# Optimization experiments

Measured on AMD Instinct MI355X. Metric: run time of the kernel, lower is better.

Reference implementation:

```python
import jax, jax.numpy as jnp
import numpy as np

N, E, D, R = 50000, 800000, 64, 65


def setup_inputs() -> dict:
    key = jax.random.key(0)
    ks = jax.random.split(key, 8)
    x = jax.random.normal(ks[0], (N, D), dtype=jnp.float32)
    src = jax.random.randint(ks[1], (E,), 0, N, dtype=jnp.int32)
    dst = jax.random.randint(ks[2], (E,), 0, N, dtype=jnp.int32)
    edge_type = jax.random.randint(ks[3], (E,), 0, R, dtype=jnp.int32)
    s = 1.0 / np.sqrt(D)
    W1 = jax.random.normal(ks[4], (R, D, D), dtype=jnp.float32) * s
    Wl1 = jax.random.normal(ks[5], (D, D), dtype=jnp.float32) * s
    W2 = jax.random.normal(ks[6], (R, D, D), dtype=jnp.float32) * s
    Wl2 = jax.random.normal(ks[7], (D, D), dtype=jnp.float32) * s
    return {"x": x, "src": src, "dst": dst, "edge_type": edge_type,
            "W1": W1, "Wl1": Wl1, "W2": W2, "Wl2": Wl2}


def _rgcn_layer(x, src, dst, edge_type, W, Wl):
    # x: [N, D_in], W: [R, D_in, D_out], Wl: [D_in, D_out]
    n = x.shape[0]
    r = W.shape[0]
    # per-relation transform of all node features: [R, N, D_out]
    xw = jnp.einsum('nd,rdh->rnh', x, W)
    # gather transformed source feature for each edge by its relation: [E, D_out]
    msg = xw[edge_type, src]
    # mean aggregation per (destination node, relation) as in PyG RGCNConv
    key = dst.astype(jnp.int32) * r + edge_type
    cnt = jax.ops.segment_sum(jnp.ones(key.shape, x.dtype), key, num_segments=n * r)
    norm = 1.0 / jnp.maximum(cnt[key], 1.0)  # [E]
    agg = jax.ops.segment_sum(msg * norm[:, None], dst, num_segments=n)  # [N, D_out]
    # self-loop linear term (self_loop_weights in original module)
    out = agg + x @ Wl
    # activation; dropout is identity in eval mode; batch norm disabled
    return jax.nn.relu(out)


def reference(x, src, dst, edge_type, W1, Wl1, W2, Wl2):
    h = _rgcn_layer(x, src, dst, edge_type, W1, Wl1)
    h = _rgcn_layer(h, src, dst, edge_type, W2, Wl2)
    return h
```

## Files before the change

kernel.cpp:

```cpp
#include <hip/hip_runtime.h>

typedef __attribute__((ext_vector_type(8))) short bf16x8;
typedef __attribute__((ext_vector_type(4))) float f32x4;

#define RFL(v) __builtin_amdgcn_readfirstlane(v)

constexpr int D = 64;
constexpr int SEG = 64;
constexpr int CSTR = 16;

__device__ inline unsigned short f2bf(float f) {
  unsigned u = __float_as_uint(f);
  u += 0x7fff + ((u >> 16) & 1);
  return (unsigned short)(u >> 16);
}
__device__ inline float bflo(unsigned u) { return __uint_as_float(u << 16); }
__device__ inline float bfhi(unsigned u) { return __uint_as_float(u & 0xffff0000u); }

__global__ __launch_bounds__(256) void count_kernel(
    const int* __restrict__ dst, const int* __restrict__ et,
    int* __restrict__ bcnt, int* __restrict__ deg, int E, int R, int nbE) {
  __shared__ int lh[128];
  int t = threadIdx.x;
  if (t < 128) lh[t] = 0;
  __syncthreads();
  int e = blockIdx.x * 256 + t;
  if (e < E) {
    atomicAdd(&deg[(long)dst[e] * CSTR], 1);
    atomicAdd(&lh[et[e]], 1);
  }
  __syncthreads();
  if (t < R) bcnt[t * nbE + blockIdx.x] = lh[t];
}

__global__ __launch_bounds__(256) void scanA_kernel(
    const int* __restrict__ arr, int* __restrict__ bsum, int n, int stride) {
  __shared__ int s[256];
  int t = threadIdx.x;
  int i = blockIdx.x * 256 + t;
  s[t] = (i < n) ? arr[(long)i * stride] : 0;
  __syncthreads();
  for (int o = 128; o > 0; o >>= 1) {
    if (t < o) s[t] += s[t + o];
    __syncthreads();
  }
  if (t == 0) bsum[blockIdx.x] = s[0];
}

__global__ __launch_bounds__(256) void scanB_kernel(int* __restrict__ bsum, int nb) {
  __shared__ int s[256];
  __shared__ int carry;
  int t = threadIdx.x;
  if (t == 0) carry = 0;
  __syncthreads();
  for (int base = 0; base < nb; base += 256) {
    int i = base + t;
    int v = (i < nb) ? bsum[i] : 0;
    s[t] = v;
    __syncthreads();
    for (int o = 1; o < 256; o <<= 1) {
      int u = (t >= o) ? s[t - o] : 0;
      __syncthreads();
      s[t] += u;
      __syncthreads();
    }
    if (i < nb) bsum[i] = carry + s[t] - v;
    __syncthreads();
    if (t == 0) carry += s[255];
    __syncthreads();
  }
}

__global__ __launch_bounds__(256) void scanC_pref_kernel(
    const int* __restrict__ arr, const int* __restrict__ bsum,
    int* __restrict__ pref, int n) {
  __shared__ int s[256];
  int t = threadIdx.x;
  int i = blockIdx.x * 256 + t;
  int v = (i < n) ? arr[i] : 0;
  s[t] = v;
  __syncthreads();
  for (int o = 1; o < 256; o <<= 1) {
    int u = (t >= o) ? s[t - o] : 0;
    __syncthreads();
    s[t] += u;
    __syncthreads();
  }
  int excl = bsum[blockIdx.x] + s[t] - v;
  if (i < n) pref[i] = excl;
  if (i == n - 1) pref[n] = excl + v;
}

__global__ __launch_bounds__(256) void scanC_deg_kernel(
    const int* __restrict__ deg, const int* __restrict__ bsum,
    int* __restrict__ dstoff, int* __restrict__ cur2, int N) {
  __shared__ int s[256];
  int t = threadIdx.x;
  int i = blockIdx.x * 256 + t;
  int v = (i < N) ? deg[(long)i * CSTR] : 0;
  s[t] = v;
  __syncthreads();
  for (int o = 1; o < 256; o <<= 1) {
    int u = (t >= o) ? s[t - o] : 0;
    __syncthreads();
    s[t] += u;
    __syncthreads();
  }
  int excl = bsum[blockIdx.x] + s[t] - v;
  if (i < N) { dstoff[i] = excl; cur2[(long)i * CSTR] = excl; }
  if (i == N - 1) dstoff[N] = excl + v;
}

__global__ void prefix_wrel_kernel(const int* __restrict__ prefE,
                                   int* __restrict__ cursor, int* __restrict__ wrel,
                                   int nbE, int R) {
  __shared__ int sc[128];
  int l = threadIdx.x;
  int c = 0;
  if (l < R) {
    int tot = prefE[(l + 1) * nbE] - prefE[l * nbE];
    c = (tot + SEG - 1) & ~(SEG - 1);
  }
  sc[l] = c;
  __syncthreads();
  for (int ofs = 1; ofs < 128; ofs <<= 1) {
    int v = (l >= ofs) ? sc[l - ofs] : 0;
    __syncthreads();
    sc[l] += v;
    __syncthreads();
  }
  if (l < R) {
    int cur = sc[l] - c;
    cursor[l] = cur;
    int w0 = cur >> 6;
    int nw = c >> 6;
    for (int w = 0; w < nw; ++w) wrel[w0 + w] = l;
  }
}

__global__ __launch_bounds__(256) void scatter_kernel(
    const int* __restrict__ src, const int* __restrict__ dst, const int* __restrict__ et,
    const int* __restrict__ cursor, const int* __restrict__ prefE,
    int* __restrict__ cur2, int2* __restrict__ eidx,
    int E, int R, int nbE) {
  __shared__ int lh[128];
  __shared__ int lbase[128];
  int t = threadIdx.x, b = blockIdx.x;
  if (t < R) {
    lh[t] = 0;
    lbase[t] = cursor[t] + prefE[t * nbE + b] - prefE[t * nbE];
  }
  __syncthreads();
  int e = b * 256 + t;
  if (e < E) {
    int r = et[e], s = src[e], d = dst[e];
    int lr = atomicAdd(&lh[r], 1);
    int jd = atomicAdd(&cur2[(long)d * CSTR], 1);
    int pos = lbase[r] + lr;
    eidx[pos] = make_int2(s, jd);
  }
}

__global__ __launch_bounds__(256) void cvt_x_kernel(
    const float* __restrict__ x, unsigned short* __restrict__ xb, int n) {
  int i = blockIdx.x * 256 + threadIdx.x;
  if (i < n) xb[i] = f2bf(x[i]);
}

__global__ __launch_bounds__(256) void cvt_w_kernel(
    const float* __restrict__ W, unsigned short* __restrict__ WT, int total) {
  int i = blockIdx.x * 256 + threadIdx.x;
  if (i >= total) return;
  int n = i & 63, k = (i >> 6) & 63, r = i >> 12;
  WT[(r << 12) + (n << 6) + k] = f2bf(W[(r << 12) + (k << 6) + n]);
}

__global__ __launch_bounds__(256)
void msg_kernel(const unsigned short* __restrict__ xb,
                const unsigned short* __restrict__ WT,
                const int2* __restrict__ eidx, const int* __restrict__ wrel,
                unsigned int* __restrict__ msgp, int* __restrict__ relrow, int nwaves) {
  const int lane = (int)threadIdx.x & 63;
  const int l15 = lane & 15;
  const int q = lane >> 4;
  const int wave = blockIdx.x * 4 + ((int)threadIdx.x >> 6);
  if (wave >= nwaves) return;
  const long base = (long)wave * SEG;
  const int r = wrel[wave];
  const unsigned short* wb = WT + ((long)r << 12);
  bf16x8 Bf[4][2];
#pragma unroll
  for (int nt = 0; nt < 4; ++nt)
#pragma unroll
    for (int kh = 0; kh < 2; ++kh)
      Bf[nt][kh] = *(const bf16x8*)(wb + (nt * 16 + l15) * 64 + kh * 32 + q * 8);
#pragma unroll
  for (int t = 0; t < 4; ++t) {
    int2 rec = eidx[base + t * 16 + l15];
    if (relrow && lane < 16 && rec.y >= 0)
      __builtin_nontemporal_store(r, &relrow[rec.y]);
    const unsigned short* xr = xb + ((long)max(rec.x, 0) << 6);
    bf16x8 A0 = *(const bf16x8*)(xr + q * 8);
    bf16x8 A1 = *(const bf16x8*)(xr + 32 + q * 8);
    f32x4 acc0 = (f32x4)0.0f, acc1 = (f32x4)0.0f, acc2 = (f32x4)0.0f, acc3 = (f32x4)0.0f;
    acc0 = __builtin_amdgcn_mfma_f32_16x16x32_bf16(A0, Bf[0][0], acc0, 0, 0, 0);
    acc0 = __builtin_amdgcn_mfma_f32_16x16x32_bf16(A1, Bf[0][1], acc0, 0, 0, 0);
    acc1 = __builtin_amdgcn_mfma_f32_16x16x32_bf16(A0, Bf[1][0], acc1, 0, 0, 0);
    acc1 = __builtin_amdgcn_mfma_f32_16x16x32_bf16(A1, Bf[1][1], acc1, 0, 0, 0);
    acc2 = __builtin_amdgcn_mfma_f32_16x16x32_bf16(A0, Bf[2][0], acc2, 0, 0, 0);
    acc2 = __builtin_amdgcn_mfma_f32_16x16x32_bf16(A1, Bf[2][1], acc2, 0, 0, 0);
    acc3 = __builtin_amdgcn_mfma_f32_16x16x32_bf16(A0, Bf[3][0], acc3, 0, 0, 0);
    acc3 = __builtin_amdgcn_mfma_f32_16x16x32_bf16(A1, Bf[3][1], acc3, 0, 0, 0);
#pragma unroll
    for (int rg = 0; rg < 4; ++rg) {
      int row = q * 4 + rg;
      int jd = __shfl(rec.y, row);
      if (jd >= 0) {
        unsigned p0 = (unsigned)f2bf(acc0[rg]) | ((unsigned)f2bf(acc1[rg]) << 16);
        unsigned p1 = (unsigned)f2bf(acc2[rg]) | ((unsigned)f2bf(acc3[rg]) << 16);
        unsigned int* mp = msgp + (long)jd * 32;
        __builtin_nontemporal_store(p0, &mp[l15]);
        __builtin_nontemporal_store(p1, &mp[16 + l15]);
      }
    }
  }
}

__global__ __launch_bounds__(256) void agg_kernel(
    const unsigned int* __restrict__ msgp, const int* __restrict__ dstoff,
    const int* __restrict__ relrow, float* __restrict__ agg, int N) {
  __shared__ int rsh[4][256];
  __shared__ float fsh[4][256];
  const int wv = (int)threadIdx.x >> 6;
  const int lane = (int)threadIdx.x & 63;
  const int j = lane & 31;
  const int half = lane >> 5;
  const int d = blockIdx.x * 4 + wv;
  if (d >= N) return;
  const int off = dstoff[d], end = dstoff[d + 1];
  const int deg = end - off;
  float aLo = 0.f, aHi = 0.f;
  if (deg > 0 && deg <= 256) {
    const int nit = (deg + 63) >> 6;
    int cl[4];
    for (int it = 0; it < nit; ++it) {
      int l = it * 64 + lane;
      if (l < deg) rsh[wv][l] = relrow[off + l];
    }
    __threadfence_block();
    for (int it = 0; it < nit; ++it) {
      int l = it * 64 + lane;
      if (l < deg) {
        int rv = rsh[wv][l];
        int c = 0;
        for (int m = 0; m < deg; ++m) c += (rsh[wv][m] == rv) ? 1 : 0;
        cl[it] = c;
      }
    }
    for (int it = 0; it < nit; ++it) {
      int l = it * 64 + lane;
      if (l < deg) fsh[wv][l] = 1.0f / (float)cl[it];
    }
    __threadfence_block();
    float a0 = 0.f, a1 = 0.f, b0 = 0.f, b1 = 0.f;
    int i = off + half;
    for (; i + 2 < end; i += 4) {
      float w0 = fsh[wv][i - off];
      float w1 = fsh[wv][i + 2 - off];
      unsigned u0 = msgp[(long)i * 32 + j];
      unsigned u1 = msgp[(long)(i + 2) * 32 + j];
      a0 = fmaf(w0, bflo(u0), a0);
      a1 = fmaf(w0, bfhi(u0), a1);
      b0 = fmaf(w1, bflo(u1), b0);
      b1 = fmaf(w1, bfhi(u1), b1);
    }
    if (i < end) {
      float w0 = fsh[wv][i - off];
      unsigned u0 = msgp[(long)i * 32 + j];
      a0 = fmaf(w0, bflo(u0), a0);
      a1 = fmaf(w0, bfhi(u0), a1);
    }
    aLo = a0 + b0;
    aHi = a1 + b1;
  } else if (deg > 256) {
    for (int i = off + half; i < end; i += 2) {
      int rv = relrow[i];
      int c = 0;
      for (int m = off; m < end; ++m) c += (relrow[m] == rv) ? 1 : 0;
      float w = 1.0f / (float)c;
      unsigned u0 = msgp[(long)i * 32 + j];
      aLo = fmaf(w, bflo(u0), aLo);
      aHi = fmaf(w, bfhi(u0), aHi);
    }
  }
  aLo += __shfl_xor(aLo, 32);
  aHi += __shfl_xor(aHi, 32);
  if (half == 0) {
    int colLo = (j < 16) ? j : j + 16;
    agg[(long)d * D + colLo] = aLo;
    agg[(long)d * D + colLo + 16] = aHi;
  }
}

__global__ __launch_bounds__(256) void selfloop_kernel(
    const unsigned short* __restrict__ xbin, const unsigned short* __restrict__ WTl,
    const float* __restrict__ agg, float* __restrict__ out,
    unsigned short* __restrict__ hb, int N) {
  const int lane = (int)threadIdx.x & 63;
  const int l15 = lane & 15;
  const int q = lane >> 4;
  const int wave = blockIdx.x * 4 + ((int)threadIdx.x >> 6);
  const int base = wave * 64;
  if (base >= N) return;
  bf16x8 Bf[4][2];
#pragma unroll
  for (int nt = 0; nt < 4; ++nt)
#pragma unroll
    for (int kh = 0; kh < 2; ++kh)
      Bf[nt][kh] = *(const bf16x8*)(WTl + (nt * 16 + l15) * 64 + kh * 32 + q * 8);
#pragma unroll
  for (int t = 0; t < 4; ++t) {
    const int row0 = base + t * 16;
    if (row0 >= N) break;
    const int m = min(row0 + l15, N - 1);
    const unsigned short* xr = xbin + ((long)m << 6);
    bf16x8 A0 = *(const bf16x8*)(xr + q * 8);
    bf16x8 A1 = *(const bf16x8*)(xr + 32 + q * 8);
    f32x4 acc[4];
#pragma unroll
    for (int nt = 0; nt < 4; ++nt) {
#pragma unroll
      for (int rg = 0; rg < 4; ++rg) {
        int node = row0 + q * 4 + rg;
        acc[nt][rg] = (node < N) ? agg[(long)node * D + nt * 16 + l15] : 0.0f;
      }
    }
#pragma unroll
    for (int nt = 0; nt < 4; ++nt) {
      acc[nt] = __builtin_amdgcn_mfma_f32_16x16x32_bf16(A0, Bf[nt][0], acc[nt], 0, 0, 0);
      acc[nt] = __builtin_amdgcn_mfma_f32_16x16x32_bf16(A1, Bf[nt][1], acc[nt], 0, 0, 0);
    }
#pragma unroll
    for (int rg = 0; rg < 4; ++rg) {
      int node = row0 + q * 4 + rg;
      if (node < N) {
#pragma unroll
        for (int nt = 0; nt < 4; ++nt) {
          float v = fmaxf(acc[nt][rg], 0.0f);
          out[(long)node * D + nt * 16 + l15] = v;
          if (hb) hb[(long)node * D + nt * 16 + l15] = f2bf(v);
        }
      }
    }
  }
}

extern "C" void kernel_launch(void* const* d_in, const int* in_sizes, int n_in,
                              void* d_out, int out_size, void* d_ws, size_t ws_size,
                              hipStream_t stream) {
  const float* x   = (const float*)d_in[0];
  const int* src   = (const int*)d_in[1];
  const int* dst   = (const int*)d_in[2];
  const int* et    = (const int*)d_in[3];
  const float* W1  = (const float*)d_in[4];
  const float* Wl1 = (const float*)d_in[5];
  const float* W2  = (const float*)d_in[6];
  const float* Wl2 = (const float*)d_in[7];
  float* out = (float*)d_out;

  const int N = in_sizes[0] / D;
  const int E = in_sizes[1];
  const int R = in_sizes[4] / (D * D);

  const int Ecap = ((E + SEG - 1) & ~(SEG - 1)) + R * SEG;
  const int nwaves = Ecap / SEG;
  const int nbN = (N + 255) / 256;
  const int nbE = (E + 255) / 256;
  const int nBC = R * nbE;
  const int nbBC = (nBC + 255) / 256;
  const int nbMax = (nbBC > nbN) ? nbBC : nbN;

  char* ws = (char*)d_ws;
  size_t off = 0;
  auto alloc = [&](size_t bytes) -> void* {
    void* p = (void*)(ws + off);
    off += (bytes + 255) & ~(size_t)255;
    return p;
  };
  int*   cursor = (int*)alloc((size_t)R * sizeof(int));
  int*   deg    = (int*)alloc((size_t)N * CSTR * sizeof(int));
  int*   cur2   = (int*)alloc((size_t)N * CSTR * sizeof(int));
  int*   bcnt   = (int*)alloc((size_t)nBC * sizeof(int));
  int*   prefE  = (int*)alloc((size_t)(nBC + 1) * sizeof(int));
  int*   bsum   = (int*)alloc((size_t)nbMax * sizeof(int));
  int*   dstoff = (int*)alloc((size_t)(N + 1) * sizeof(int));
  int*   relrow = (int*)alloc((size_t)E * sizeof(int));
  int*   wrel   = (int*)alloc((size_t)nwaves * sizeof(int));
  int2*  eidx   = (int2*)alloc((size_t)(Ecap + SEG) * sizeof(int2));
  unsigned int* msgp = (unsigned int*)alloc((size_t)E * 32 * sizeof(unsigned int));
  float* agg    = (float*)alloc((size_t)N * D * sizeof(float));
  unsigned short* xb  = (unsigned short*)alloc((size_t)N * D * sizeof(unsigned short));
  unsigned short* hb  = (unsigned short*)alloc((size_t)N * D * sizeof(unsigned short));
  unsigned short* WT1 = (unsigned short*)alloc((size_t)R * D * D * sizeof(unsigned short));
  unsigned short* WT2 = (unsigned short*)alloc((size_t)R * D * D * sizeof(unsigned short));
  unsigned short* WTl1 = (unsigned short*)alloc((size_t)D * D * sizeof(unsigned short));
  unsigned short* WTl2 = (unsigned short*)alloc((size_t)D * D * sizeof(unsigned short));
  (void)ws_size; (void)n_in; (void)out_size;

  const int msg_blocks = (nwaves + 3) / 4;
  const int agg_blocks = (N + 3) / 4;
  const int sl_waves = (N + 63) / 64;
  const int sl_blocks = (sl_waves + 3) / 4;
  const int wtot = R * D * D;

  hipMemsetAsync(deg, 0, (size_t)N * CSTR * sizeof(int), stream);
  hipMemsetAsync(wrel, 0, (size_t)nwaves * sizeof(int), stream);
  hipMemsetAsync(eidx, 0xFF, (size_t)(Ecap + SEG) * sizeof(int2), stream);
  count_kernel<<<nbE, 256, 0, stream>>>(dst, et, bcnt, deg, E, R, nbE);
  scanA_kernel<<<nbBC, 256, 0, stream>>>(bcnt, bsum, nBC, 1);
  scanB_kernel<<<1, 256, 0, stream>>>(bsum, nbBC);
  scanC_pref_kernel<<<nbBC, 256, 0, stream>>>(bcnt, bsum, prefE, nBC);
  prefix_wrel_kernel<<<1, 128, 0, stream>>>(prefE, cursor, wrel, nbE, R);
  scanA_kernel<<<nbN, 256, 0, stream>>>(deg, bsum, N, CSTR);
  scanB_kernel<<<1, 256, 0, stream>>>(bsum, nbN);
  scanC_deg_kernel<<<nbN, 256, 0, stream>>>(deg, bsum, dstoff, cur2, N);
  scatter_kernel<<<nbE, 256, 0, stream>>>(src, dst, et, cursor, prefE, cur2,
                                          eidx, E, R, nbE);
  cvt_x_kernel<<<(N * D + 255) / 256, 256, 0, stream>>>(x, xb, N * D);
  cvt_w_kernel<<<(wtot + 255) / 256, 256, 0, stream>>>(W1, WT1, wtot);
  cvt_w_kernel<<<(wtot + 255) / 256, 256, 0, stream>>>(W2, WT2, wtot);
  cvt_w_kernel<<<(D * D + 255) / 256, 256, 0, stream>>>(Wl1, WTl1, D * D);
  cvt_w_kernel<<<(D * D + 255) / 256, 256, 0, stream>>>(Wl2, WTl2, D * D);

  msg_kernel<<<msg_blocks, 256, 0, stream>>>(xb, WT1, eidx, wrel, msgp, relrow, nwaves);
  agg_kernel<<<agg_blocks, 256, 0, stream>>>(msgp, dstoff, relrow, agg, N);
  selfloop_kernel<<<sl_blocks, 256, 0, stream>>>(xb, WTl1, agg, out, hb, N);

  msg_kernel<<<msg_blocks, 256, 0, stream>>>(hb, WT2, eidx, wrel, msgp, nullptr, nwaves);
  agg_kernel<<<agg_blocks, 256, 0, stream>>>(msgp, dstoff, relrow, agg, N);
  selfloop_kernel<<<sl_blocks, 256, 0, stream>>>(hb, WTl2, agg, out, nullptr, N);
}
```

Baseline: 376.0 us.

## Fuse aggregation with self-loop GEMM and merge preprocessing launches

```diff
diff --git a/kernel.cpp b/kernel.cpp
--- a/kernel.cpp
+++ b/kernel.cpp
@@ -2,12 +2,11 @@
 
 typedef __attribute__((ext_vector_type(8))) short bf16x8;
 typedef __attribute__((ext_vector_type(4))) float f32x4;
-
-#define RFL(v) __builtin_amdgcn_readfirstlane(v)
 
 constexpr int D = 64;
 constexpr int SEG = 64;
 constexpr int CSTR = 16;
+constexpr int TSTR = 68;
 
 __device__ inline unsigned short f2bf(float f) {
   unsigned u = __float_as_uint(f);
@@ -33,24 +32,32 @@
   if (t < R) bcnt[t * nbE + blockIdx.x] = lh[t];
 }
 
-__global__ __launch_bounds__(256) void scanA_kernel(
-    const int* __restrict__ arr, int* __restrict__ bsum, int n, int stride) {
+__global__ __launch_bounds__(256) void scanA_dual_kernel(
+    const int* __restrict__ bcnt, const int* __restrict__ deg,
+    int* __restrict__ bsum, int nBC, int N, int nbBC) {
   __shared__ int s[256];
   int t = threadIdx.x;
-  int i = blockIdx.x * 256 + t;
-  s[t] = (i < n) ? arr[(long)i * stride] : 0;
+  int b = blockIdx.x;
+  int v;
+  if (b < nbBC) {
+    int i = b * 256 + t;
+    v = (i < nBC) ? bcnt[i] : 0;
+  } else {
+    int i = (b - nbBC) * 256 + t;
+    v = (i < N) ? deg[(long)i * CSTR] : 0;
+  }
+  s[t] = v;
   __syncthreads();
   for (int o = 128; o > 0; o >>= 1) {
     if (t < o) s[t] += s[t + o];
     __syncthreads();
   }
-  if (t == 0) bsum[blockIdx.x] = s[0];
-}
-
-__global__ __launch_bounds__(256) void scanB_kernel(int* __restrict__ bsum, int nb) {
+  if (t == 0) bsum[b] = s[0];
+}
+
+__device__ inline void scanB_region(int* bsum, int nb, int t) {
   __shared__ int s[256];
   __shared__ int carry;
-  int t = threadIdx.x;
   if (t == 0) carry = 0;
   __syncthreads();
   for (int base = 0; base < nb; base += 256) {
@@ -71,13 +78,26 @@
   }
 }
 
-__global__ __launch_bounds__(256) void scanC_pref_kernel(
-    const int* __restrict__ arr, const int* __restrict__ bsum,
-    int* __restrict__ pref, int n) {
+__global__ __launch_bounds__(256) void scanB_dual_kernel(
+    int* __restrict__ bsum, int nbBC, int nbN) {
+  int t = threadIdx.x;
+  scanB_region(bsum, nbBC, t);
+  scanB_region(bsum + nbBC, nbN, t);
+}
+
+__global__ __launch_bounds__(256) void scanC_dual_kernel(
+    const int* __restrict__ bcnt, const int* __restrict__ deg,
+    const int* __restrict__ bsum, int* __restrict__ prefE,
+    int* __restrict__ dstoff, int* __restrict__ cur2,
+    int nBC, int N, int nbBC) {
   __shared__ int s[256];
   int t = threadIdx.x;
-  int i = blockIdx.x * 256 + t;
-  int v = (i < n) ? arr[i] : 0;
+  int b = blockIdx.x;
+  bool isBC = (b < nbBC);
+  int i = (isBC ? b : b - nbBC) * 256 + t;
+  int n = isBC ? nBC : N;
+  int v = 0;
+  if (i < n) v = isBC ? bcnt[i] : deg[(long)i * CSTR];
   s[t] = v;
   __syncthreads();
   for (int o = 1; o < 256; o <<= 1) {
@@ -86,29 +106,14 @@
     s[t] += u;
     __syncthreads();
   }
-  int excl = bsum[blockIdx.x] + s[t] - v;
-  if (i < n) pref[i] = excl;
-  if (i == n - 1) pref[n] = excl + v;
-}
-
-__global__ __launch_bounds__(256) void scanC_deg_kernel(
-    const int* __restrict__ deg, const int* __restrict__ bsum,
-    int* __restrict__ dstoff, int* __restrict__ cur2, int N) {
-  __shared__ int s[256];
-  int t = threadIdx.x;
-  int i = blockIdx.x * 256 + t;
-  int v = (i < N) ? deg[(long)i * CSTR] : 0;
-  s[t] = v;
-  __syncthreads();
-  for (int o = 1; o < 256; o <<= 1) {
-    int u = (t >= o) ? s[t - o] : 0;
-    __syncthreads();
-    s[t] += u;
-    __syncthreads();
-  }
-  int excl = bsum[blockIdx.x] + s[t] - v;
-  if (i < N) { dstoff[i] = excl; cur2[(long)i * CSTR] = excl; }
-  if (i == N - 1) dstoff[N] = excl + v;
+  int excl = bsum[b] + s[t] - v;
+  if (isBC) {
+    if (i < n) prefE[i] = excl;
+    if (i == n - 1) prefE[n] = excl + v;
+  } else {
+    if (i < n) { dstoff[i] = excl; cur2[(long)i * CSTR] = excl; }
+    if (i == n - 1) dstoff[n] = excl + v;
+  }
 }
 
 __global__ void prefix_wrel_kernel(const int* __restrict__ prefE,
@@ -161,21 +166,34 @@
   }
 }
 
-__global__ __launch_bounds__(256) void cvt_x_kernel(
-    const float* __restrict__ x, unsigned short* __restrict__ xb, int n) {
+__global__ __launch_bounds__(256) void cvt_all_kernel(
+    const float* __restrict__ x, unsigned short* __restrict__ xb, int nx,
+    const float* __restrict__ W1, unsigned short* __restrict__ WT1,
+    const float* __restrict__ W2, unsigned short* __restrict__ WT2, int nw,
+    const float* __restrict__ Wl1, unsigned short* __restrict__ WTl1,
+    const float* __restrict__ Wl2, unsigned short* __restrict__ WTl2, int nl) {
   int i = blockIdx.x * 256 + threadIdx.x;
-  if (i < n) xb[i] = f2bf(x[i]);
-}
-
-__global__ __launch_bounds__(256) void cvt_w_kernel(
-    const float* __restrict__ W, unsigned short* __restrict__ WT, int total) {
-  int i = blockIdx.x * 256 + threadIdx.x;
-  if (i >= total) return;
-  int n = i & 63, k = (i >> 6) & 63, r = i >> 12;
-  WT[(r << 12) + (n << 6) + k] = f2bf(W[(r << 12) + (k << 6) + n]);
-}
-
-__global__ __launch_bounds__(256)
+  if (i < nx) { xb[i] = f2bf(x[i]); return; }
+  i -= nx;
+  if (i < 2 * nw) {
+    const float* W = (i < nw) ? W1 : W2;
+    unsigned short* WT = (i < nw) ? WT1 : WT2;
+    int i2 = (i < nw) ? i : i - nw;
+    int n = i2 & 63, k = (i2 >> 6) & 63, r = i2 >> 12;
+    WT[(r << 12) + (n << 6) + k] = f2bf(W[(r << 12) + (k << 6) + n]);
+    return;
+  }
+  i -= 2 * nw;
+  if (i < 2 * nl) {
+    const float* W = (i < nl) ? Wl1 : Wl2;
+    unsigned short* WT = (i < nl) ? WTl1 : WTl2;
+    int i2 = (i < nl) ? i : i - nl;
+    int n = i2 & 63, k = (i2 >> 6) & 63;
+    WT[(n << 6) + k] = f2bf(W[(k << 6) + n]);
+  }
+}
+
+__global__ __launch_bounds__(256) __attribute__((amdgpu_waves_per_eu(1, 4)))
 void msg_kernel(const unsigned short* __restrict__ xb,
                 const unsigned short* __restrict__ WT,
                 const int2* __restrict__ eidx, const int* __restrict__ wrel,
@@ -197,8 +215,7 @@
 #pragma unroll
   for (int t = 0; t < 4; ++t) {
     int2 rec = eidx[base + t * 16 + l15];
-    if (relrow && lane < 16 && rec.y >= 0)
-      __builtin_nontemporal_store(r, &relrow[rec.y]);
+    if (relrow && lane < 16 && rec.y >= 0) relrow[rec.y] = r;
     const unsigned short* xr = xb + ((long)max(rec.x, 0) << 6);
     bf16x8 A0 = *(const bf16x8*)(xr + q * 8);
     bf16x8 A1 = *(const bf16x8*)(xr + 32 + q * 8);
@@ -219,137 +236,129 @@
         unsigned p0 = (unsigned)f2bf(acc0[rg]) | ((unsigned)f2bf(acc1[rg]) << 16);
         unsigned p1 = (unsigned)f2bf(acc2[rg]) | ((unsigned)f2bf(acc3[rg]) << 16);
         unsigned int* mp = msgp + (long)jd * 32;
-        __builtin_nontemporal_store(p0, &mp[l15]);
-        __builtin_nontemporal_store(p1, &mp[16 + l15]);
+        mp[l15] = p0;
+        mp[16 + l15] = p1;
       }
     }
   }
 }
 
-__global__ __launch_bounds__(256) void agg_kernel(
+__global__ __launch_bounds__(256) void aggself_kernel(
     const unsigned int* __restrict__ msgp, const int* __restrict__ dstoff,
-    const int* __restrict__ relrow, float* __restrict__ agg, int N) {
+    const int* __restrict__ relrow, const unsigned short* __restrict__ xbin,
+    const unsigned short* __restrict__ WTl, float* __restrict__ out,
+    unsigned short* __restrict__ hb, int N) {
+  __shared__ float tile[4][16 * TSTR];
   __shared__ int rsh[4][256];
   __shared__ float fsh[4][256];
   const int wv = (int)threadIdx.x >> 6;
   const int lane = (int)threadIdx.x & 63;
   const int j = lane & 31;
   const int half = lane >> 5;
-  const int d = blockIdx.x * 4 + wv;
-  if (d >= N) return;
-  const int off = dstoff[d], end = dstoff[d + 1];
-  const int deg = end - off;
-  float aLo = 0.f, aHi = 0.f;
-  if (deg > 0 && deg <= 256) {
-    const int nit = (deg + 63) >> 6;
-    int cl[4];
-    for (int it = 0; it < nit; ++it) {
-      int l = it * 64 + lane;
-      if (l < deg) rsh[wv][l] = relrow[off + l];
-    }
-    __threadfence_block();
-    for (int it = 0; it < nit; ++it) {
-      int l = it * 64 + lane;
-      if (l < deg) {
-        int rv = rsh[wv][l];
-        int c = 0;
-        for (int m = 0; m < deg; ++m) c += (rsh[wv][m] == rv) ? 1 : 0;
-        cl[it] = c;
+  const int l15 = lane & 15;
+  const int q = lane >> 4;
+  const int base = blockIdx.x * 64 + wv * 16;
+  bf16x8 Bf[4][2];
+#pragma unroll
+  for (int nt = 0; nt < 4; ++nt)
+#pragma unroll
+    for (int kh = 0; kh < 2; ++kh)
+      Bf[nt][kh] = *(const bf16x8*)(WTl + (nt * 16 + l15) * 64 + kh * 32 + q * 8);
+  if (base >= N) return;
+  for (int k = 0; k < 16; ++k) {
+    int d = base + k;
+    float aLo = 0.f, aHi = 0.f;
+    if (d < N) {
+      const int off = dstoff[d], end = dstoff[d + 1];
+      const int deg = end - off;
+      if (deg > 0 && deg <= 256) {
+        const int nit = (deg + 63) >> 6;
+        int cl[4];
+        for (int it = 0; it < nit; ++it) {
+          int l = it * 64 + lane;
+          if (l < deg) rsh[wv][l] = relrow[off + l];
+        }
+        __threadfence_block();
+        for (int it = 0; it < nit; ++it) {
+          int l = it * 64 + lane;
+          if (l < deg) {
+            int rv = rsh[wv][l];
+            int c = 0;
+            for (int m = 0; m < deg; ++m) c += (rsh[wv][m] == rv) ? 1 : 0;
+            cl[it] = c;
+          }
+        }
+        for (int it = 0; it < nit; ++it) {
+          int l = it * 64 + lane;
+          if (l < deg) fsh[wv][l] = 1.0f / (float)cl[it];
+        }
+        __threadfence_block();
+        float a0 = 0.f, a1 = 0.f, b0 = 0.f, b1 = 0.f;
+        int i = off + half;
+        for (; i + 2 < end; i += 4) {
+          float w0 = fsh[wv][i - off];
+          float w1 = fsh[wv][i + 2 - off];
+          unsigned u0 = msgp[(long)i * 32 + j];
+          unsigned u1 = msgp[(long)(i + 2) * 32 + j];
+          a0 = fmaf(w0, bflo(u0), a0);
+          a1 = fmaf(w0, bfhi(u0), a1);
+          b0 = fmaf(w1, bflo(u1), b0);
+          b1 = fmaf(w1, bfhi(u1), b1);
+        }
+        if (i < end) {
+          float w0 = fsh[wv][i - off];
+          unsigned u0 = msgp[(long)i * 32 + j];
+          a0 = fmaf(w0, bflo(u0), a0);
+          a1 = fmaf(w0, bfhi(u0), a1);
+        }
+        aLo = a0 + b0;
+        aHi = a1 + b1;
+      } else if (deg > 256) {
+        for (int i = off + half; i < end; i += 2) {
+          int rv = relrow[i];
+          int c = 0;
+          for (int m = off; m < end; ++m) c += (relrow[m] == rv) ? 1 : 0;
+          float w = 1.0f / (float)c;
+          unsigned u0 = msgp[(long)i * 32 + j];
+          aLo = fmaf(w, bflo(u0), aLo);
+          aHi = fmaf(w, bfhi(u0), aHi);
+        }
       }
     }
-    for (int it = 0; it < nit; ++it) {
-      int l = it * 64 + lane;
-      if (l < deg) fsh[wv][l] = 1.0f / (float)cl[it];
+    aLo += __shfl_xor(aLo, 32);
+    aHi += __shfl_xor(aHi, 32);
+    if (half == 0) {
+      int colLo = (j < 16) ? j : j + 16;
+      tile[wv][k * TSTR + colLo] = aLo;
+      tile[wv][k * TSTR + colLo + 16] = aHi;
     }
-    __threadfence_block();
-    float a0 = 0.f, a1 = 0.f, b0 = 0.f, b1 = 0.f;
-    int i = off + half;
-    for (; i + 2 < end; i += 4) {
-      float w0 = fsh[wv][i - off];
-      float w1 = fsh[wv][i + 2 - off];
-      unsigned u0 = msgp[(long)i * 32 + j];
-      unsigned u1 = msgp[(long)(i + 2) * 32 + j];
-      a0 = fmaf(w0, bflo(u0), a0);
-      a1 = fmaf(w0, bfhi(u0), a1);
-      b0 = fmaf(w1, bflo(u1), b0);
-      b1 = fmaf(w1, bfhi(u1), b1);
-    }
-    if (i < end) {
-      float w0 = fsh[wv][i - off];
-      unsigned u0 = msgp[(long)i * 32 + j];
-      a0 = fmaf(w0, bflo(u0), a0);
-      a1 = fmaf(w0, bfhi(u0), a1);
-    }
-    aLo = a0 + b0;
-    aHi = a1 + b1;
-  } else if (deg > 256) {
-    for (int i = off + half; i < end; i += 2) {
-      int rv = relrow[i];
-      int c = 0;
-      for (int m = off; m < end; ++m) c += (relrow[m] == rv) ? 1 : 0;
-      float w = 1.0f / (float)c;
-      unsigned u0 = msgp[(long)i * 32 + j];
-      aLo = fmaf(w, bflo(u0), aLo);
-      aHi = fmaf(w, bfhi(u0), aHi);
-    }
-  }
-  aLo += __shfl_xor(aLo, 32);
-  aHi += __shfl_xor(aHi, 32);
-  if (half == 0) {
-    int colLo = (j < 16) ? j : j + 16;
-    agg[(long)d * D + colLo] = aLo;
-    agg[(long)d * D + colLo + 16] = aHi;
-  }
-}
-
-__global__ __launch_bounds__(256) void selfloop_kernel(
-    const unsigned short* __restrict__ xbin, const unsigned short* __restrict__ WTl,
-    const float* __restrict__ agg, float* __restrict__ out,
-    unsigned short* __restrict__ hb, int N) {
-  const int lane = (int)threadIdx.x & 63;
-  const int l15 = lane & 15;
-  const int q = lane >> 4;
-  const int wave = blockIdx.x * 4 + ((int)threadIdx.x >> 6);
-  const int base = wave * 64;
-  if (base >= N) return;
-  bf16x8 Bf[4][2];
-#pragma unroll
-  for (int nt = 0; nt < 4; ++nt)
-#pragma unroll
-    for (int kh = 0; kh < 2; ++kh)
-      Bf[nt][kh] = *(const bf16x8*)(WTl + (nt * 16 + l15) * 64 + kh * 32 + q * 8);
-#pragma unroll
-  for (int t = 0; t < 4; ++t) {
-    const int row0 = base + t * 16;
-    if (row0 >= N) break;
-    const int m = min(row0 + l15, N - 1);
-    const unsigned short* xr = xbin + ((long)m << 6);
-    bf16x8 A0 = *(const bf16x8*)(xr + q * 8);
-    bf16x8 A1 = *(const bf16x8*)(xr + 32 + q * 8);
-    f32x4 acc[4];
-#pragma unroll
-    for (int nt = 0; nt < 4; ++nt) {
-#pragma unroll
-      for (int rg = 0; rg < 4; ++rg) {
-        int node = row0 + q * 4 + rg;
-        acc[nt][rg] = (node < N) ? agg[(long)node * D + nt * 16 + l15] : 0.0f;
-      }
-    }
-#pragma unroll
-    for (int nt = 0; nt < 4; ++nt) {
-      acc[nt] = __builtin_amdgcn_mfma_f32_16x16x32_bf16(A0, Bf[nt][0], acc[nt], 0, 0, 0);
-      acc[nt] = __builtin_amdgcn_mfma_f32_16x16x32_bf16(A1, Bf[nt][1], acc[nt], 0, 0, 0);
-    }
-#pragma unroll
-    for (int rg = 0; rg < 4; ++rg) {
-      int node = row0 + q * 4 + rg;
-      if (node < N) {
-#pragma unroll
-        for (int nt = 0; nt < 4; ++nt) {
-          float v = fmaxf(acc[nt][rg], 0.0f);
-          out[(long)node * D + nt * 16 + l15] = v;
-          if (hb) hb[(long)node * D + nt * 16 + l15] = f2bf(v);
-        }
+  }
+  __threadfence_block();
+  const int m = min(base + l15, N - 1);
+  const unsigned short* xr = xbin + ((long)m << 6);
+  bf16x8 A0 = *(const bf16x8*)(xr + q * 8);
+  bf16x8 A1 = *(const bf16x8*)(xr + 32 + q * 8);
+  f32x4 acc[4];
+#pragma unroll
+  for (int nt = 0; nt < 4; ++nt) {
+#pragma unroll
+    for (int rg = 0; rg < 4; ++rg)
+      acc[nt][rg] = tile[wv][(q * 4 + rg) * TSTR + nt * 16 + l15];
+  }
+#pragma unroll
+  for (int nt = 0; nt < 4; ++nt) {
+    acc[nt] = __builtin_amdgcn_mfma_f32_16x16x32_bf16(A0, Bf[nt][0], acc[nt], 0, 0, 0);
+    acc[nt] = __builtin_amdgcn_mfma_f32_16x16x32_bf16(A1, Bf[nt][1], acc[nt], 0, 0, 0);
+  }
+#pragma unroll
+  for (int rg = 0; rg < 4; ++rg) {
+    int node = base + q * 4 + rg;
+    if (node < N) {
+#pragma unroll
+      for (int nt = 0; nt < 4; ++nt) {
+        float v = fmaxf(acc[nt][rg], 0.0f);
+        out[(long)node * D + nt * 16 + l15] = v;
+        if (hb) hb[(long)node * D + nt * 16 + l15] = f2bf(v);
       }
     }
   }
@@ -378,7 +387,6 @@
   const int nbE = (E + 255) / 256;
   const int nBC = R * nbE;
   const int nbBC = (nBC + 255) / 256;
-  const int nbMax = (nbBC > nbN) ? nbBC : nbN;
 
   char* ws = (char*)d_ws;
   size_t off = 0;
@@ -392,13 +400,12 @@
   int*   cur2   = (int*)alloc((size_t)N * CSTR * sizeof(int));
   int*   bcnt   = (int*)alloc((size_t)nBC * sizeof(int));
   int*   prefE  = (int*)alloc((size_t)(nBC + 1) * sizeof(int));
-  int*   bsum   = (int*)alloc((size_t)nbMax * sizeof(int));
+  int*   bsum   = (int*)alloc((size_t)(nbBC + nbN) * sizeof(int));
   int*   dstoff = (int*)alloc((size_t)(N + 1) * sizeof(int));
   int*   relrow = (int*)alloc((size_t)E * sizeof(int));
   int*   wrel   = (int*)alloc((size_t)nwaves * sizeof(int));
   int2*  eidx   = (int2*)alloc((size_t)(Ecap + SEG) * sizeof(int2));
   unsigned int* msgp = (unsigned int*)alloc((size_t)E * 32 * sizeof(unsigned int));
-  float* agg    = (float*)alloc((size_t)N * D * sizeof(float));
   unsigned short* xb  = (unsigned short*)alloc((size_t)N * D * sizeof(unsigned short));
   unsigned short* hb  = (unsigned short*)alloc((size_t)N * D * sizeof(unsigned short));
   unsigned short* WT1 = (unsigned short*)alloc((size_t)R * D * D * sizeof(unsigned short));
@@ -408,35 +415,30 @@
   (void)ws_size; (void)n_in; (void)out_size;
 
   const int msg_blocks = (nwaves + 3) / 4;
-  const int agg_blocks = (N + 3) / 4;
-  const int sl_waves = (N + 63) / 64;
-  const int sl_blocks = (sl_waves + 3) / 4;
-  const int wtot = R * D * D;
+  const int as_blocks = (N + 63) / 64;
+  const int nx = N * D;
+  const int nw = R * D * D;
+  const int nl = D * D;
+  const int cvt_total = nx + 2 * nw + 2 * nl;
 
   hipMemsetAsync(deg, 0, (size_t)N * CSTR * sizeof(int), stream);
   hipMemsetAsync(wrel, 0, (size_t)nwaves * sizeof(int), stream);
   hipMemsetAsync(eidx, 0xFF, (size_t)(Ecap + SEG) * sizeof(int2), stream);
   count_kernel<<<nbE, 256, 0, stream>>>(dst, et, bcnt, deg, E, R, nbE);
-  scanA_kernel<<<nbBC, 256, 0, stream>>>(bcnt, bsum, nBC, 1);
-  scanB_kernel<<<1, 256, 0, stream>>>(bsum, nbBC);
-  scanC_pref_kernel<<<nbBC, 256, 0, stream>>>(bcnt, bsum, prefE, nBC);
+  scanA_dual_kernel<<<nbBC + nbN, 256, 0, stream>>>(bcnt, deg, bsum, nBC, N, nbBC);
+  scanB_dual_kernel<<<1, 256, 0, stream>>>(bsum, nbBC, nbN);
+  scanC_dual_kernel<<<nbBC + nbN, 256, 0, stream>>>(bcnt, deg, bsum, prefE,
+                                                    dstoff, cur2, nBC, N, nbBC);
   prefix_wrel_kernel<<<1, 128, 0, stream>>>(prefE, cursor, wrel, nbE, R);
-  scanA_kernel<<<nbN, 256, 0, stream>>>(deg, bsum, N, CSTR);
-  scanB_kernel<<<1, 256, 0, stream>>>(bsum, nbN);
-  scanC_deg_kernel<<<nbN, 256, 0, stream>>>(deg, bsum, dstoff, cur2, N);
   scatter_kernel<<<nbE, 256, 0, stream>>>(src, dst, et, cursor, prefE, cur2,
                                           eidx, E, R, nbE);
-  cvt_x_kernel<<<(N * D + 255) / 256, 256, 0, stream>>>(x, xb, N * D);
-  cvt_w_kernel<<<(wtot + 255) / 256, 256, 0, stream>>>(W1, WT1, wtot);
-  cvt_w_kernel<<<(wtot + 255) / 256, 256, 0, stream>>>(W2, WT2, wtot);
-  cvt_w_kernel<<<(D * D + 255) / 256, 256, 0, stream>>>(Wl1, WTl1, D * D);
-  cvt_w_kernel<<<(D * D + 255) / 256, 256, 0, stream>>>(Wl2, WTl2, D * D);
+  cvt_all_kernel<<<(cvt_total + 255) / 256, 256, 0, stream>>>(
+      x, xb, nx, W1, WT1, W2, WT2, nw, Wl1, WTl1, Wl2, WTl2, nl);
 
   msg_kernel<<<msg_blocks, 256, 0, stream>>>(xb, WT1, eidx, wrel, msgp, relrow, nwaves);
-  agg_kernel<<<agg_blocks, 256, 0, stream>>>(msgp, dstoff, relrow, agg, N);
-  selfloop_kernel<<<sl_blocks, 256, 0, stream>>>(xb, WTl1, agg, out, hb, N);
-
+  aggself_kernel<<<as_blocks, 256, 0, stream>>>(msgp, dstoff, relrow, xb, WTl1,
+                                                out, hb, N);
   msg_kernel<<<msg_blocks, 256, 0, stream>>>(hb, WT2, eidx, wrel, msgp, nullptr, nwaves);
-  agg_kernel<<<agg_blocks, 256, 0, stream>>>(msgp, dstoff, relrow, agg, N);
-  selfloop_kernel<<<sl_blocks, 256, 0, stream>>>(hb, WTl2, agg, out, nullptr, N);
-}
+  aggself_kernel<<<as_blocks, 256, 0, stream>>>(msgp, dstoff, relrow, hb, WTl2,
+                                                out, nullptr, N);
+}
```

Measured after the change: 392.6 us. 1.04x slower.
